# Performance work log

Measured on AMD Instinct MI355X. Metric: run time of the kernel, lower is better.

Reference implementation:

```python
import jax, jax.numpy as jnp
import numpy as np

# distilgpt2 dims
D, NH, HD, NL, V, FF = 768, 12, 64, 6, 50258, 3072
# st-moe dims: Expert hidden = int(768*4*2/3) = 2048 (GEGLU -> first linear out = 4096)
E, TOPN, MOE_H = 8, 2, 2048
CAPF, THRESH, MINCAP, EPS = 1.25, 0.2, 4, 1e-9
BAL_COEF, Z_COEF = 0.01, 0.001
ROUTE_KEY = jax.random.key(1234)  # deterministic stand-in for torch's in-forward uniform_ routing noise


def layer_norm(x, g, b):
    m = jnp.mean(x, -1, keepdims=True)
    v = jnp.mean(jnp.square(x - m), -1, keepdims=True)
    return (x - m) * jax.lax.rsqrt(v + 1e-5) * g + b


def rms_norm(x, g):
    # st-moe RMSNorm: F.normalize(x, dim=-1) * sqrt(dim) * gamma
    n = jnp.sqrt(jnp.sum(jnp.square(x), -1, keepdims=True))
    return x / jnp.maximum(n, 1e-12) * (D ** 0.5) * g


def geglu(h, mult_bias):
    a, gate = jnp.split(h, 2, -1)
    return a * jax.nn.gelu(gate, approximate=False) * mult_bias


def st_ff(x, p):
    # Expert(prenorm=True): RMSNorm -> Linear -> GEGLU -> Linear
    norm_g, w1, b1, mb, w2, b2 = p
    h = rms_norm(x, norm_g)
    return geglu(h @ w1 + b1, mb) @ w2 + b2


def causal_attn(x, wqkv, bqkv, wo, bo):
    B, S, _ = x.shape
    q, k, v = jnp.split(x @ wqkv + bqkv, 3, -1)
    sh = lambda t: t.reshape(B, S, NH, HD).transpose(0, 2, 1, 3)
    q, k, v = sh(q), sh(k), sh(v)
    att = jnp.einsum('bhqd,bhkd->bhqk', q, k) / (HD ** 0.5)
    causal = jnp.tril(jnp.ones((S, S), bool))
    att = jax.nn.softmax(jnp.where(causal, att, jnp.finfo(att.dtype).min), -1)
    o = jnp.einsum('bhqk,bhkd->bhqd', att, v).transpose(0, 2, 1, 3).reshape(B, S, D)
    return o @ wo + bo


def gpt2_mlp(x, wfc, bfc, wproj, bproj):
    # GPT2 uses gelu_new (tanh approximation)
    return jax.nn.gelu(x @ wfc + bfc, approximate=True) @ wproj + bproj


def top_n_gating(x, gate_w, key):
    b, n, _ = x.shape
    cap = max(min(n, int(n * CAPF / E)), MINCAP)
    logits = x @ gate_w                                    # (b,n,E)
    raw = jax.nn.softmax(logits, -1)
    gv, gi = jax.lax.top_k(raw, TOPN)
    gates = jnp.moveaxis(gv, -1, 0)                        # (k,b,n)
    one_hot = jax.nn.one_hot(jnp.moveaxis(gi, -1, 0), E, dtype=x.dtype)  # (k,b,n,E)
    mask1 = one_hot[0]
    gates = gates / jnp.clip(jnp.sum(gates, 0, keepdims=True), EPS)
    thr = jnp.array([EPS, THRESH], x.dtype).reshape(TOPN, 1, 1)
    probs = jax.random.uniform(key, gates.shape, x.dtype)
    route = (probs < gates / thr).at[0].set(True)          # always route to top-1 expert
    mask = one_hot * route[..., None].astype(x.dtype)
    cums = jnp.cumsum(mask, -2) - mask                     # exclusive cumsum over seq
    prev = jnp.zeros((b, 1, E), x.dtype)
    positions, masks = [], []
    for kk in range(TOPN):
        pos = (cums[kk] + prev) * mask[kk]                 # (b,n,E) slot within expert
        mk = mask[kk] * (pos < cap).astype(x.dtype)        # drop overflow beyond capacity
        prev = prev + jnp.sum(mk, -2, keepdims=True)
        positions.append(jnp.sum(pos, -1))                 # (b,n)
        masks.append(mk)
    positions = jnp.stack(positions)                       # (k,b,n)
    mask = jnp.stack(masks)                                # (k,b,n,E)
    mask_flat = jnp.sum(mask, -1)                          # (k,b,n)
    gm = gates * mask_flat * mask_flat
    pos_oh = jax.nn.one_hot(positions.astype(jnp.int32), cap, dtype=x.dtype)  # safe one-hot: OOR -> 0
    combine = jnp.einsum('kbn,kbne,kbnc->bnec', gm, one_hot, pos_oh)
    hard = (combine > 0).astype(x.dtype)
    dispatch = hard + combine - jax.lax.stop_gradient(combine)  # straight-through dispatch
    balance = jnp.mean(jnp.mean(raw, -2) * jnp.mean(mask1, -2)) * float(E ** 2)
    zloss = jnp.mean(jnp.square(jax.nn.logsumexp(logits, -1)))
    return dispatch, combine, balance, zloss


def moe_block(x, ffb, ffa, moe_norm_g, gate_w, ep, key):
    x = st_ff(x, ffb) + x
    res = x
    h = rms_norm(x, moe_norm_g)
    dispatch, combine, bal, zloss = top_n_gating(h, gate_w, key)
    ein = jnp.einsum('bnd,bnec->ebcd', h, dispatch)        # dispatch tokens to experts
    expert = lambda inp, w1, b1, mb, w2, b2: geglu(inp @ w1 + b1, mb) @ w2 + b2
    eout = jax.vmap(expert)(ein, *ep)                      # (E,b,c,d)
    mo = jnp.einsum('ebcd,bnec->bnd', eout, combine)       # weighted combine
    x = mo + res
    x = st_ff(x, ffa) + x
    return x, BAL_COEF * bal + Z_COEF * zloss


def forward(input_ids, wte, wpe, ln1_g, ln1_b, ln2_g, ln2_b, aw, ab, apw, apb, mfw, mfb, mpw, mpb, lnf_g, lnf_b, ffb, ffa, moe_norm_g, gate_w, ep):
    B, S = input_ids.shape
    out = wte[input_ids] + wpe[:S]
    aux = jnp.zeros((), out.dtype)
    for i in range(NL):
        out = out + causal_attn(layer_norm(out, ln1_g[i], ln1_b[i]), aw[i], ab[i], apw[i], apb[i])
        h = layer_norm(out, ln2_g[i], ln2_b[i])
        if i in (0, 3):  # shared SparseMoEBlock replaces MLP (original computes-and-discards the MLP)
            ffo, a = moe_block(h, ffb, ffa, moe_norm_g, gate_w, ep, jax.random.fold_in(ROUTE_KEY, i))
            aux = aux + a
        else:
            ffo = gpt2_mlp(h, mfw[i], mfb[i], mpw[i], mpb[i])
        out = out + ffo
    out = layer_norm(out, lnf_g, lnf_b)
    return out @ wte.T, aux  # tied lm_head


def setup_inputs():
    key = jax.random.key(0)
    ks = iter(jax.random.split(key, 40))
    w = lambda *s: jax.random.normal(next(ks), s, jnp.float32) * 0.02
    B, S = 2, 512
    return dict(
        input_ids=jax.random.randint(next(ks), (B, S), 0, V, jnp.int32),
        attention_mask=jnp.ones((B, S), jnp.int32),
        wte=w(V, D), wpe=w(1024, D),
        ln1_g=jnp.ones((NL, D)), ln1_b=jnp.zeros((NL, D)),
        ln2_g=jnp.ones((NL, D)), ln2_b=jnp.zeros((NL, D)),
        attn_qkv_w=w(NL, D, 3 * D), attn_qkv_b=jnp.zeros((NL, 3 * D)),
        attn_proj_w=w(NL, D, D), attn_proj_b=jnp.zeros((NL, D)),
        mlp_fc_w=w(NL, D, FF), mlp_fc_b=jnp.zeros((NL, FF)),
        mlp_proj_w=w(NL, FF, D), mlp_proj_b=jnp.zeros((NL, D)),
        lnf_g=jnp.ones((D,)), lnf_b=jnp.zeros((D,)),
        ffb_norm_g=jnp.ones((D,)), ffb_w1=w(D, 2 * MOE_H), ffb_b1=jnp.zeros((2 * MOE_H,)), ffb_mb=jnp.ones((MOE_H,)), ffb_w2=w(MOE_H, D), ffb_b2=jnp.zeros((D,)),
        ffa_norm_g=jnp.ones((D,)), ffa_w1=w(D, 2 * MOE_H), ffa_b1=jnp.zeros((2 * MOE_H,)), ffa_mb=jnp.ones((MOE_H,)), ffa_w2=w(MOE_H, D), ffa_b2=jnp.zeros((D,)),
        moe_norm_g=jnp.ones((D,)), gate_w=w(D, E),
        exp_w1=w(E, D, 2 * MOE_H), exp_b1=jnp.zeros((E, 2 * MOE_H)), exp_mb=jnp.ones((E, MOE_H)), exp_w2=w(E, MOE_H, D), exp_b2=jnp.zeros((E, D)),
    )


def reference(input_ids, attention_mask, wte, wpe, ln1_g, ln1_b, ln2_g, ln2_b, attn_qkv_w, attn_qkv_b, attn_proj_w, attn_proj_b, mlp_fc_w, mlp_fc_b, mlp_proj_w, mlp_proj_b, lnf_g, lnf_b, ffb_norm_g, ffb_w1, ffb_b1, ffb_mb, ffb_w2, ffb_b2, ffa_norm_g, ffa_w1, ffa_b1, ffa_mb, ffa_w2, ffa_b2, moe_norm_g, gate_w, exp_w1, exp_b1, exp_mb, exp_w2, exp_b2):
    # attention_mask is built but never used by the original forward (causal-only attention)
    del attention_mask
    return forward(input_ids, wte, wpe, ln1_g, ln1_b, ln2_g, ln2_b,
                   attn_qkv_w, attn_qkv_b, attn_proj_w, attn_proj_b,
                   mlp_fc_w, mlp_fc_b, mlp_proj_w, mlp_proj_b, lnf_g, lnf_b,
                   (ffb_norm_g, ffb_w1, ffb_b1, ffb_mb, ffb_w2, ffb_b2),
                   (ffa_norm_g, ffa_w1, ffa_b1, ffa_mb, ffa_w2, ffa_b2),
                   moe_norm_g, gate_w, (exp_w1, exp_b1, exp_mb, exp_w2, exp_b2))
```

## Files before the change

kernel.cpp:

```cpp
#include <hip/hip_runtime.h>
#include <cstdint>

#define DD     768
#define NTOK   1024
#define SEQ    512
#define NHEAD  12
#define HDIM   64
#define VOCAB  50258
#define CAP    80
#define AUXOFF 51464192LL

typedef short bf16x8 __attribute__((ext_vector_type(8)));
typedef float f32x4  __attribute__((ext_vector_type(4)));

__host__ __device__ inline void threefry(uint32_t k0, uint32_t k1,
                                         uint32_t& x0, uint32_t& x1) {
  uint32_t ks0 = k0, ks1 = k1, ks2 = k0 ^ k1 ^ 0x1BD11BDAu;
  x0 += ks0; x1 += ks1;
#define RND(r) { x0 += x1; x1 = (x1 << (r)) | (x1 >> (32 - (r))); x1 ^= x0; }
  RND(13) RND(15) RND(26) RND(6)   x0 += ks1; x1 += ks2 + 1u;
  RND(17) RND(29) RND(16) RND(24)  x0 += ks2; x1 += ks0 + 2u;
  RND(13) RND(15) RND(26) RND(6)   x0 += ks0; x1 += ks1 + 3u;
  RND(17) RND(29) RND(16) RND(24)  x0 += ks1; x1 += ks2 + 4u;
  RND(13) RND(15) RND(26) RND(6)   x0 += ks2; x1 += ks0 + 5u;
// ... 7 lines not shown
}
__device__ inline float bf2f(unsigned short h) {
  union { uint32_t u; float f; } v; v.u = ((uint32_t)h) << 16; return v.f;
}
__device__ inline float gelu_tanh_f(float x) {
  float x3 = x * x * x;
  return 0.5f * x * (1.f + tanhf(0.7978845608028654f * (x + 0.044715f * x3)));
}
__device__ inline float gelu_erf_f(float x) {
  return 0.5f * x * (1.f + erff(x * 0.7071067811865476f));
}

template<bool TRANS_B>
__global__ __launch_bounds__(256)
void k_gemm(const float* __restrict__ Ag, const float* __restrict__ Bg,
            float* __restrict__ Cg, const float* __restrict__ biasg,
            const float* __restrict__ residg,
            int M, int N, int K, int lda, int ldb, int ldc, int nh,
            long long sAb, long long sAh, long long sBb, long long sBh,
            long long sCb, long long sCh, long long sBias, int act)
{
  const int z  = blockIdx.z;
  const int zb = z / nh, zh = z - zb * nh;
  const float* A = Ag + zb * sAb + zh * sAh;
  const float* B = Bg + zb * sBb + zh * sBh;
  float*       C = Cg + zb * sCb + zh * sCh;
  const float* R = residg ? residg + zb * sCb + zh * sCh : nullptr;
  const float* bs = biasg ? biasg + (long long)z * sBias : nullptr;

  const int m0 = blockIdx.y * 64;
  const int n0 = blockIdx.x * 64;

  __shared__ __attribute__((aligned(16))) unsigned short sAh_[64][36];
  __shared__ __attribute__((aligned(16))) unsigned short sAl_[64][36];
  __shared__ __attribute__((aligned(16))) unsigned short sBh_[64][36];
  __shared__ __attribute__((aligned(16))) unsigned short sBl_[64][36];

  const int tid  = threadIdx.x;
  const int wave = tid >> 6;
  const int lane = tid & 63;
  const int l15  = lane & 15;
  const int kf   = (lane >> 4) * 8;
// ... 78 lines not shown
    __syncthreads();
  }

  #pragma unroll
  for (int f = 0; f < 4; f++) {
    int col = n0 + f * 16 + l15;
    if (col >= N) continue;
    float bv = bs ? bs[col] : 0.f;
    #pragma unroll
    for (int i = 0; i < 4; i++) {
      int row = m0 + wave * 16 + (lane >> 4) * 4 + i;
      if (row >= M) continue;
      float v = acc[f][i] + bv;
      if (act == 1) v = gelu_tanh_f(v);
      if (R) v += R[(long long)row * ldc + col];
      C[(long long)row * ldc + col] = v;
    }
  }
}

__global__ __launch_bounds__(256)
void k_gemmw(const float* __restrict__ Ag, const unsigned short* __restrict__ Bhg,
             const unsigned short* __restrict__ Blg, float* __restrict__ Cg,
             const float* __restrict__ biasg, const float* __restrict__ residg,
             int M, int N, int K, int ldc,
             long long sAz, long long sBz, long long sCz, long long sBias,
             int act, int swz)
{
  const int z = blockIdx.z;
  const float* A = Ag + z * sAz;
  const unsigned short* BH = Bhg + z * sBz;
  const unsigned short* BL = Blg + z * sBz;
  float* C = Cg + z * sCz;
  const float* R = residg ? residg + z * sCz : nullptr;
  const float* bs = biasg ? biasg + z * sBias : nullptr;

  int xt, yt;
  if (swz) {
    int gx = gridDim.x, gy = gridDim.y;
    int bid = blockIdx.y * gx + blockIdx.x;
    int nblk = gx * gy;
    int q = nblk >> 3, r = nblk & 7;
    int xcd = bid & 7, idx = bid >> 3;
    int nl = (xcd < r ? xcd * (q + 1) : r * (q + 1) + (xcd - r) * q) + idx;
    yt = nl % gy; xt = nl / gy;
  } else { xt = blockIdx.x; yt = blockIdx.y; }

  const int m0 = yt * 64, n0 = xt * 128;
// ... 3 lines not shown
  __shared__ __attribute__((aligned(16))) unsigned short sBh[128][40];
  __shared__ __attribute__((aligned(16))) unsigned short sBl[128][40];

  const int tid = threadIdx.x, wave = tid >> 6, lane = tid & 63;
  const int l15 = lane & 15, kf = (lane >> 4) * 8;
  const int wr = (wave >> 1) * 32, wc = (wave & 1) * 64;

  f32x4 zf = {0.f, 0.f, 0.f, 0.f};
  f32x4 acc[2][4] = {{zf, zf, zf, zf}, {zf, zf, zf, zf}};

  const int ar = tid >> 2, ac = (tid & 3) * 8;
  const int br = tid >> 1, bc = (tid & 1) * 16;

  for (int kk = 0; kk < K; kk += 32) {
    {
      float v[8];
      if (m0 + ar < M) {
        const float* p = A + (long long)(m0 + ar) * K + kk + ac;
        #pragma unroll
        for (int j = 0; j < 8; j++) v[j] = p[j];
      } else {
        #pragma unroll
        for (int j = 0; j < 8; j++) v[j] = 0.f;
      }
      #pragma unroll
      for (int j = 0; j < 8; j += 4) {
        unsigned short h0 = f2bf(v[j]),     h1 = f2bf(v[j + 1]);
        unsigned short h2 = f2bf(v[j + 2]), h3 = f2bf(v[j + 3]);
        uint2 ph, pl;
        ph.x = (uint32_t)h0 | ((uint32_t)h1 << 16);
        ph.y = (uint32_t)h2 | ((uint32_t)h3 << 16);
        pl.x = (uint32_t)f2bf(v[j] - bf2f(h0))     | ((uint32_t)f2bf(v[j + 1] - bf2f(h1)) << 16);
        pl.y = (uint32_t)f2bf(v[j + 2] - bf2f(h2)) | ((uint32_t)f2bf(v[j + 3] - bf2f(h3)) << 16);
        *(uint2*)&sAh[ar][ac + j] = ph;
        *(uint2*)&sAl[ar][ac + j] = pl;
      }
    }
    {
      int nrow = n0 + br;
      if (nrow < N) {
        const uint4* ph = (const uint4*)(BH + (long long)nrow * K + kk + bc);
        const uint4* pl = (const uint4*)(BL + (long long)nrow * K + kk + bc);
        *(uint4*)&sBh[br][bc]     = ph[0];
        *(uint4*)&sBh[br][bc + 8] = ph[1];
        *(uint4*)&sBl[br][bc]     = pl[0];
        *(uint4*)&sBl[br][bc + 8] = pl[1];
      } else {
        uint4 z4 = {0, 0, 0, 0};
        *(uint4*)&sBh[br][bc] = z4; *(uint4*)&sBh[br][bc + 8] = z4;
        *(uint4*)&sBl[br][bc] = z4; *(uint4*)&sBl[br][bc + 8] = z4;
// ... 12 lines not shown
    #pragma unroll
    for (int j = 0; j < 4; j++) {
      union { uint4 q; bf16x8 v; } ub, ulb;
      ub.q  = *(const uint4*)&sBh[wc + j * 16 + l15][kf];
      ulb.q = *(const uint4*)&sBl[wc + j * 16 + l15][kf];
      #pragma unroll
      for (int i = 0; i < 2; i++) {
        acc[i][j] = __builtin_amdgcn_mfma_f32_16x16x32_bf16(ah[i], ub.v,  acc[i][j], 0, 0, 0);
        acc[i][j] = __builtin_amdgcn_mfma_f32_16x16x32_bf16(al[i], ub.v,  acc[i][j], 0, 0, 0);
        acc[i][j] = __builtin_amdgcn_mfma_f32_16x16x32_bf16(ah[i], ulb.v, acc[i][j], 0, 0, 0);
      }
    }
    __syncthreads();
  }

  #pragma unroll
  for (int j = 0; j < 4; j++) {
    int col = n0 + wc + j * 16 + l15;
    if (col >= N) continue;
    float bv = bs ? bs[col] : 0.f;
    #pragma unroll
    for (int i = 0; i < 2; i++) {
      #pragma unroll
      for (int rr = 0; rr < 4; rr++) {
        int row = m0 + wr + i * 16 + (lane >> 4) * 4 + rr;
        if (row >= M) continue;
        float v = acc[i][j][rr] + bv;
        if (act == 1) v = gelu_tanh_f(v);
        if (R) v += R[(long long)row * ldc + col];
        C[(long long)row * ldc + col] = v;
      }
    }
  }
}

__global__ void k_split(const float* __restrict__ src, unsigned short* __restrict__ dh,
                        unsigned short* __restrict__ dl, long long n) {
  long long i = ((long long)blockIdx.x * 256 + threadIdx.x) * 4;
  if (i >= n) return;
  float4 v = *(const float4*)(src + i);
  float vv[4] = {v.x, v.y, v.z, v.w};
  unsigned short h[4], l[4];
  #pragma unroll
  for (int j = 0; j < 4; j++) {
    h[j] = f2bf(vv[j]);
// ... 26 lines not shown
  }
}

__global__ void k_embed(const int* __restrict__ ids, const float* __restrict__ wte,
                        const float* __restrict__ wpe, float* __restrict__ X) {
  int t = blockIdx.x; int s = t & (SEQ - 1);
  long long wb = (long long)ids[t] * DD;
  #pragma unroll
  for (int i = 0; i < 3; i++) {
    int d = threadIdx.x + 256 * i;
    X[(long long)t * DD + d] = wte[wb + d] + wpe[(long long)s * DD + d];
  }
}

__global__ void k_layernorm(const float* __restrict__ in, const float* __restrict__ g,
                            const float* __restrict__ b, float* __restrict__ out) {
  int t = blockIdx.x; int lane = threadIdx.x;
  float xv[12]; float s = 0.f, ss = 0.f;
  #pragma unroll
  for (int i = 0; i < 12; i++) {
    xv[i] = in[(long long)t * DD + lane + 64 * i];
    s += xv[i]; ss += xv[i] * xv[i];
  }
  for (int o = 32; o; o >>= 1) { s += __shfl_xor(s, o); ss += __shfl_xor(ss, o); }
  float mean = s * (1.f / DD);
  float var  = ss * (1.f / DD) - mean * mean;
  float rst  = rsqrtf(var + 1e-5f);
  #pragma unroll
  for (int i = 0; i < 12; i++) {
    int d = lane + 64 * i;
    out[(long long)t * DD + d] = (xv[i] - mean) * rst * g[d] + b[d];
  }
}

__global__ void k_rmsnorm(const float* __restrict__ in, const float* __restrict__ g,
                          float* __restrict__ out) {
  int t = blockIdx.x; int lane = threadIdx.x;
  float xv[12]; float ss = 0.f;
  #pragma unroll
  for (int i = 0; i < 12; i++) {
    xv[i] = in[(long long)t * DD + lane + 64 * i];
    ss += xv[i] * xv[i];
  }
  for (int o = 32; o; o >>= 1) ss += __shfl_xor(ss, o);
  float scale = 27.712812921102035f / fmaxf(sqrtf(ss), 1e-12f);
  #pragma unroll
  for (int i = 0; i < 12; i++) {
    int d = lane + 64 * i;
    out[(long long)t * DD + d] = xv[i] * scale * g[d];
  }
}

__global__ void k_softmax(float* __restrict__ S) {
  int r = blockIdx.x; int q = r & (SEQ - 1);
  float* p = S + (long long)r * SEQ;
  int lane = threadIdx.x;
  float v[8]; float mx = -3.4e38f;
  #pragma unroll
  for (int i = 0; i < 8; i++) {
    int j = lane + 64 * i;
    v[i] = p[j] * 0.125f;
    if (j <= q) mx = fmaxf(mx, v[i]);
  }
  for (int o = 32; o; o >>= 1) mx = fmaxf(mx, __shfl_xor(mx, o));
  float s = 0.f;
  #pragma unroll
  for (int i = 0; i < 8; i++) {
    int j = lane + 64 * i;
    float e = (j <= q) ? expf(v[i] - mx) : 0.f;
    v[i] = e; s += e;
  }
  for (int o = 32; o; o >>= 1) s += __shfl_xor(s, o);
  float inv = 1.f / s;
  #pragma unroll
  for (int i = 0; i < 8; i++) p[lane + 64 * i] = v[i] * inv;
}

__global__ void k_geglu(const float* __restrict__ in, const float* __restrict__ mb,
                        float* __restrict__ out, int rows_per_mb) {
  int row = blockIdx.x;
  const float* mbp = mb + (long long)(row / rows_per_mb) * 2048;
  #pragma unroll
  for (int i = 0; i < 8; i++) {
    int j = threadIdx.x + 256 * i;
    float a = in[(long long)row * 4096 + j];
    float g = in[(long long)row * 4096 + 2048 + j];
    out[(long long)row * 2048 + j] = a * gelu_erf_f(g) * mbp[j];
  }
}

__global__ void k_zero(float* __restrict__ p, int n) {
  int i = blockIdx.x * blockDim.x + threadIdx.x;
  if (i < n) p[i] = 0.f;
}

__global__ void k_add(float* __restrict__ X, const float* __restrict__ Y, int n) {
  int i = blockIdx.x * 256 + threadIdx.x;
  if (i < n) X[i] += Y[i];
}

__global__ void k_gate(const float* __restrict__ RB, const float* __restrict__ GW,
                       unsigned int fk0, unsigned int fk1,
// ... 38 lines not shown
    uint32_t x0 = (uint32_t)t, x1 = (uint32_t)t + 1024u;
    threefry(fk0, fk1, x0, x1);
    union { uint32_t u; float f; } uf; uf.u = (x1 >> 9) | 0x3f800000u;
    float u = uf.f - 1.f;
    int r1 = (u < g1 * 5.f) ? 1 : 0;
    e0a[t] = e0; e1a[t] = e1; g0a[t] = g0; g1a[t] = g1; r1a[t] = r1;
    atomicAdd(&cnt1[b * 8 + e0], 1.f);
    atomicAdd(lse2, lse * lse);
  }
}

__global__ void k_scan(const int* __restrict__ e0a, const int* __restrict__ e1a,
                       const int* __restrict__ r1a,
                       int* __restrict__ s0a, int* __restrict__ s1a,
                       int* __restrict__ ts) {
  int tid = threadIdx.x;
  if (tid >= 16) return;
  int b = tid >> 3, e = tid & 7;
  int base = (e * 2 + b) * CAP;
  for (int c = 0; c < CAP; c++) ts[base + c] = -1;
  int c0 = 0;
  for (int n = 0; n < SEQ; n++) {
    int t = b * SEQ + n;
    if (e0a[t] == e) {
      if (c0 < CAP) { s0a[t] = c0; ts[base + c0] = t; } else s0a[t] = -1;
      c0++;
    }
  }
  int prev = c0 < CAP ? c0 : CAP;
  int c1 = 0;
  for (int n = 0; n < SEQ; n++) {
    int t = b * SEQ + n;
    if (e1a[t] == e) {
      if (r1a[t]) {
        int pos = prev + c1;
        if (pos < CAP) { s1a[t] = pos; ts[base + pos] = t; } else s1a[t] = -1;
        c1++;
      } else s1a[t] = -1;
    }
  }
}

__global__ void k_dispatch(const float* __restrict__ RB, const int* __restrict__ ts,
                           float* __restrict__ EIN) {
  int s = blockIdx.x;
  int t = ts[s];
  #pragma unroll
  for (int i = 0; i < 3; i++) {
    int d = threadIdx.x + 256 * i;
    EIN[(long long)s * DD + d] = (t >= 0) ? RB[(long long)t * DD + d] : 0.f;
  }
}

__global__ void k_combine(const int* __restrict__ e0a, const int* __restrict__ e1a,
                          const int* __restrict__ s0a, const int* __restrict__ s1a,
                          const float* __restrict__ g0a, const float* __restrict__ g1a,
                          const float* __restrict__ EOUT, float* __restrict__ XM) {
  int t = blockIdx.x; int b = t >> 9;
  int s0 = s0a[t], s1 = s1a[t];
  long long r0 = ((long long)e0a[t] * 160 + b * CAP + s0) * DD;
  long long r1 = ((long long)e1a[t] * 160 + b * CAP + s1) * DD;
  float g0 = g0a[t], g1 = g1a[t];
  #pragma unroll
  for (int i = 0; i < 3; i++) {
    int d = threadIdx.x + 256 * i;
// ... 45 lines not shown
  const float* ffaw1 = (const float*)d_in[25];
  const float* ffab1 = (const float*)d_in[26];
  const float* ffamb = (const float*)d_in[27];
  const float* ffaw2 = (const float*)d_in[28];
  const float* ffab2 = (const float*)d_in[29];
  const float* moeng = (const float*)d_in[30];
  const float* gw    = (const float*)d_in[31];
  const float* ew1   = (const float*)d_in[32];
  const float* eb1   = (const float*)d_in[33];
  const float* emb   = (const float*)d_in[34];
  const float* ew2   = (const float*)d_in[35];
  const float* eb2   = (const float*)d_in[36];

  float* ws = (float*)d_ws;
  float* X    = ws + 0;
  float* LN   = ws + 786432;
  float* RB   = ws + 1572864;
  float* XM   = ws + 2359296;
  float* QKV  = ws + 3145728;
  float* BIG  = ws + 5505024;
  float* GB   = ws + 11796480;
  float* EIN  = ws + 14417920;
  float* EOUT = ws + 15400960;
  float* MISC = ws + 16384000;
  int*   e0a = (int*)MISC;
  int*   e1a = e0a + 1024;
  int*   s0a = e1a + 1024;
  int*   s1a = s0a + 1024;
  int*   r1a = s1a + 1024;
  float* g0a = (float*)(r1a + 1024);
  float* g1a = g0a + 1024;
  int*   tsa = (int*)(g1a + 1024);
  float* sum_raw = (float*)(tsa + 1280);
  float* cnt1 = sum_raw + 16;
  float* lse2 = cnt1 + 16;

  float* logits = (float*)d_out;
  float* aux = logits + AUXOFF;

  const long long E_wte = 38598144LL, E_qkv = 1769472LL, E_apr = 589824LL;
  const long long E_fc = 2359296LL, E_mpr = 2359296LL;
  const long long E_fb1 = 3145728LL, E_fb2 = 1572864LL;
  const long long E_ew1 = 3145728LL, E_ew2 = 1572864LL;
  const long long o_wte = 0;
  const long long o_qkv = o_wte + 2 * E_wte;
  const long long o_apr = o_qkv + 12 * E_qkv;
  const long long o_fc  = o_apr + 12 * E_apr;
  const long long o_mpr = o_fc  + 8 * E_fc;
  const long long o_fb1 = o_mpr + 8 * E_mpr;
  const long long o_fb2 = o_fb1 + 2 * E_fb1;
  const long long o_fa1 = o_fb2 + 2 * E_fb2;
  const long long o_fa2 = o_fa1 + 2 * E_fb1;
  const long long o_ew1 = o_fa2 + 2 * E_fb2;
  const long long o_ew2 = o_ew1 + 16 * E_ew1;
  const long long o_end = o_ew2 + 16 * E_ew2;
  unsigned short* SP = (unsigned short*)(ws + 16400000);
  const bool useSplit = ((long long)ws_size >= 16400000LL * 4 + o_end * 2);

  unsigned int fk[2][2];
  { uint32_t a = 0, b = 0; threefry(0u, 1234u, a, b); fk[0][0] = a; fk[0][1] = b; }
  { uint32_t a = 0, b = 3; threefry(0u, 1234u, a, b); fk[1][0] = a; fk[1][1] = b; }

  auto gemm = [&](bool transB, const float* A, const float* Bm, float* Cm,
                  const float* bias, const float* resid,
                  int M, int N, int K, int lda, int ldb, int ldc,
                  int batches, int nh,
                  long long sAb, long long sAh, long long sBb, long long sBh,
                  long long sCb, long long sCh, long long sBias, int act) {
    dim3 g((N + 63) / 64, (M + 63) / 64, batches);
    if (transB)
      k_gemm<true><<<g, 256, 0, stream>>>(A, Bm, Cm, bias, resid, M, N, K, lda, ldb, ldc,
                                          nh, sAb, sAh, sBb, sBh, sCb, sCh, sBias, act);
    else
      k_gemm<false><<<g, 256, 0, stream>>>(A, Bm, Cm, bias, resid, M, N, K, lda, ldb, ldc,
                                           nh, sAb, sAh, sBb, sBh, sCb, sCh, sBias, act);
  };

  auto wgemm = [&](const float* A, const float* Bf, long long bOff, long long bE,
                   float* Cm, const float* bias, const float* resid,
                   int M, int N, int K, int ldc, int nz,
                   long long sAz, long long sBf, long long sCz, long long sBias,
                   int act, int swz) {
    if (useSplit) {
      dim3 g((N + 127) / 128, (M + 63) / 64, nz);
      k_gemmw<<<g, 256, 0, stream>>>(A, SP + bOff, SP + bOff + bE, Cm, bias, resid,
                                     M, N, K, ldc, sAz, 2 * bE, sCz, sBias, act, swz);
    } else {
      gemm(false, A, Bf, Cm, bias, resid, M, N, K, K, N, ldc,
           nz, 1, sAz, 0, sBf, 0, sCz, 0, sBias, act);
    }
  };

  if (useSplit) {
    auto splitT = [&](const float* src, long long dOff, long long E, int K_, int N_,
                      int nz, long long sSrc) {
      k_split_t<<<dim3(N_ / 32, K_ / 32, nz), 256, 0, stream>>>(
          src, SP + dOff, SP + dOff + E, K_, N_, sSrc, 2 * E);
    };
    k_split<<<(int)((E_wte / 4 + 255) / 256), 256, 0, stream>>>(
        wte, SP + o_wte, SP + o_wte + E_wte, E_wte);
    splitT(aqw, o_qkv, E_qkv, 768, 2304, 6, 768LL * 2304);
    splitT(apw, o_apr, E_apr, 768, 768, 6, 768LL * 768);
    int mlpLayers[4] = {1, 2, 4, 5};
    for (int s = 0; s < 4; s++) {
      int L = mlpLayers[s];
      splitT(mfw + (long long)L * E_fc,  o_fc  + s * 2 * E_fc,  E_fc,  768, 3072, 1, 0);
      splitT(mpw + (long long)L * E_mpr, o_mpr + s * 2 * E_mpr, E_mpr, 3072, 768, 1, 0);
    }
    splitT(ffbw1, o_fb1, E_fb1, 768, 4096, 1, 0);
    splitT(ffbw2, o_fb2, E_fb2, 2048, 768, 1, 0);
    splitT(ffaw1, o_fa1, E_fb1, 768, 4096, 1, 0);
    splitT(ffaw2, o_fa2, E_fb2, 2048, 768, 1, 0);
    splitT(ew1, o_ew1, E_ew1, 768, 4096, 8, (long long)768 * 4096);
    splitT(ew2, o_ew2, E_ew2, 2048, 768, 8, (long long)2048 * 768);
  }

  auto moe = [&](unsigned int fk0, unsigned int fk1) {
    k_rmsnorm<<<1024, 64, 0, stream>>>(LN, ffbng, RB);
    wgemm(RB, ffbw1, o_fb1, E_fb1, BIG, ffbb1, nullptr,
          1024, 4096, 768, 4096, 1, 0, 0, 0, 0, 0, 1);
    k_geglu<<<1024, 256, 0, stream>>>(BIG, ffbmb, GB, 1024);
    wgemm(GB, ffbw2, o_fb2, E_fb2, XM, ffbb2, LN,
          1024, 768, 2048, 768, 1, 0, 0, 0, 0, 0, 1);
    k_rmsnorm<<<1024, 64, 0, stream>>>(XM, moeng, RB);
    k_zero<<<1, 64, 0, stream>>>(sum_raw, 33);
    k_gate<<<1024, 64, 0, stream>>>(RB, gw, fk0, fk1, e0a, e1a, g0a, g1a, r1a,
                                    sum_raw, cnt1, lse2);
    k_scan<<<1, 64, 0, stream>>>(e0a, e1a, r1a, s0a, s1a, tsa);
    k_dispatch<<<1280, 256, 0, stream>>>(RB, tsa, EIN);
    wgemm(EIN, ew1, o_ew1, E_ew1, BIG, eb1, nullptr,
          160, 4096, 768, 4096, 8, 122880, 3145728, 655360, 4096, 0, 0);
    k_geglu<<<1280, 256, 0, stream>>>(BIG, emb, GB, 160);
    wgemm(GB, ew2, o_ew2, E_ew2, EOUT, eb2, nullptr,
          160, 768, 2048, 768, 8, 327680, 1572864, 122880, 768, 0, 0);
    k_combine<<<1024, 256, 0, stream>>>(e0a, e1a, s0a, s1a, g0a, g1a, EOUT, XM);
    k_aux<<<1, 1, 0, stream>>>(sum_raw, cnt1, lse2, aux);
    k_rmsnorm<<<1024, 64, 0, stream>>>(XM, ffang, RB);
    wgemm(RB, ffaw1, o_fa1, E_fb1, BIG, ffab1, nullptr,
          1024, 4096, 768, 4096, 1, 0, 0, 0, 0, 0, 1);
    k_geglu<<<1024, 256, 0, stream>>>(BIG, ffamb, GB, 1024);
    wgemm(GB, ffaw2, o_fa2, E_fb2, XM, ffab2, XM,
          1024, 768, 2048, 768, 1, 0, 0, 0, 0, 0, 1);
    k_add<<<3072, 256, 0, stream>>>(X, XM, 786432);
  };

  k_zero<<<1, 64, 0, stream>>>(aux, 1);
  k_embed<<<1024, 256, 0, stream>>>(ids, wte, wpe, X);

  for (int i = 0; i < 6; i++) {
    k_layernorm<<<1024, 64, 0, stream>>>(X, ln1g + i * 768, ln1b + i * 768, LN);
    wgemm(LN, aqw + (long long)i * 768 * 2304, o_qkv + (long long)i * 2 * E_qkv, E_qkv,
          QKV, aqb + (long long)i * 2304, nullptr,
          1024, 2304, 768, 2304, 1, 0, 0, 0, 0, 0, 1);
    gemm(true, QKV, QKV + 768, BIG, nullptr, nullptr, 512, 512, 64, 2304, 2304, 512,
         24, 12, 1179648, 64, 1179648, 64, 3145728, 262144, 0, 0);
    k_softmax<<<12288, 64, 0, stream>>>(BIG);
    gemm(false, BIG, QKV + 1536, GB, nullptr, nullptr, 512, 64, 512, 512, 2304, 768,
         24, 12, 3145728, 262144, 1179648, 64, 393216, 64, 0, 0);
    wgemm(GB, apw + (long long)i * 768 * 768, o_apr + (long long)i * 2 * E_apr, E_apr,
          X, apb + (long long)i * 768, X,
          1024, 768, 768, 768, 1, 0, 0, 0, 0, 0, 1);
    k_layernorm<<<1024, 64, 0, stream>>>(X, ln2g + i * 768, ln2b + i * 768, LN);
    if (i == 0 || i == 3) {
      moe(fk[i == 0 ? 0 : 1][0], fk[i == 0 ? 0 : 1][1]);
    } else {
      int slot = (i < 3) ? (i - 1) : (i - 2);
      wgemm(LN, mfw + (long long)i * 768 * 3072, o_fc + (long long)slot * 2 * E_fc, E_fc,
            BIG, mfb + (long long)i * 3072, nullptr,
            1024, 3072, 768, 3072, 1, 0, 0, 0, 0, 1, 1);
      wgemm(BIG, mpw + (long long)i * 3072 * 768, o_mpr + (long long)slot * 2 * E_mpr, E_mpr,
            X, mpb + (long long)i * 768, X,
            1024, 768, 3072, 768, 1, 0, 0, 0, 0, 0, 1);
    }
  }

  k_layernorm<<<1024, 64, 0, stream>>>(X, lnfg, lnfb, LN);
  if (useSplit) {
    wgemm(LN, nullptr, o_wte, E_wte, logits, nullptr, nullptr,
          1024, VOCAB, 768, VOCAB, 1, 0, 0, 0, 0, 0, 1);
  } else {
    gemm(true, LN, wte, logits, nullptr, nullptr, 1024, VOCAB, 768, 768, 768, VOCAB,
         1, 1, 0, 0, 0, 0, 0, 0, 0, 0);
  }
}
```

Measured before the change: 4.412 ms.

## Emit pre-split bf16 hi/lo activations from producers to skip GEMM A-side conversion

Result: faster. 4.134 ms (-6.3%).

```diff
diff --git a/kernel.cpp b/kernel.cpp
--- a/kernel.cpp
+++ b/kernel.cpp
@@ -45,18 +45,19 @@
 template<bool TRANS_B>
 __global__ __launch_bounds__(256)
 void k_gemm(const float* __restrict__ Ag, const float* __restrict__ Bg,
-            float* __restrict__ Cg, const float* __restrict__ biasg,
-            const float* __restrict__ residg,
+            float* __restrict__ Cg, unsigned short* __restrict__ Chg,
+            unsigned short* __restrict__ Clg,
+            const float* __restrict__ biasg, const float* __restrict__ residg,
             int M, int N, int K, int lda, int ldb, int ldc, int nh,
             long long sAb, long long sAh, long long sBb, long long sBh,
-            long long sCb, long long sCh, long long sBias, int act)
+            long long sCb, long long sCh, long long sBias, int act, int osplit)
 {
   const int z  = blockIdx.z;
   const int zb = z / nh, zh = z - zb * nh;
   const float* A = Ag + zb * sAb + zh * sAh;
   const float* B = Bg + zb * sBb + zh * sBh;
-  float*       C = Cg + zb * sCb + zh * sCh;
-  const float* R = residg ? residg + zb * sCb + zh * sCh : nullptr;
+  const long long cOff = zb * sCb + zh * sCh;
+  const float* R = residg ? residg + cOff : nullptr;
   const float* bs = biasg ? biasg + (long long)z * sBias : nullptr;
 
   const int m0 = blockIdx.y * 64;
@@ -165,24 +166,33 @@
       float v = acc[f][i] + bv;
       if (act == 1) v = gelu_tanh_f(v);
       if (R) v += R[(long long)row * ldc + col];
-      C[(long long)row * ldc + col] = v;
+      long long idx = cOff + (long long)row * ldc + col;
+      if (osplit) {
+        unsigned short h = f2bf(v);
+        Chg[idx] = h;
+        Clg[idx] = f2bf(v - bf2f(h));
+      } else {
+        Cg[idx] = v;
+      }
     }
   }
 }
 
 __global__ __launch_bounds__(256)
-void k_gemmw(const float* __restrict__ Ag, const unsigned short* __restrict__ Bhg,
-             const unsigned short* __restrict__ Blg, float* __restrict__ Cg,
+void k_gemmw(const unsigned short* __restrict__ Ahg, const unsigned short* __restrict__ Alg,
+             const unsigned short* __restrict__ Bhg, const unsigned short* __restrict__ Blg,
+             float* __restrict__ Cg, unsigned short* __restrict__ Chg,
+             unsigned short* __restrict__ Clg,
              const float* __restrict__ biasg, const float* __restrict__ residg,
              int M, int N, int K, int ldc,
              long long sAz, long long sBz, long long sCz, long long sBias,
              int act, int swz)
 {
   const int z = blockIdx.z;
-  const float* A = Ag + z * sAz;
+  const unsigned short* AH = Ahg + z * sAz;
+  const unsigned short* AL = Alg + z * sAz;
   const unsigned short* BH = Bhg + z * sBz;
   const unsigned short* BL = Blg + z * sBz;
-  float* C = Cg + z * sCz;
   const float* R = residg ? residg + z * sCz : nullptr;
   const float* bs = biasg ? biasg + z * sBias : nullptr;
 
@@ -216,26 +226,14 @@
 
   for (int kk = 0; kk < K; kk += 32) {
     {
-      float v[8];
       if (m0 + ar < M) {
-        const float* p = A + (long long)(m0 + ar) * K + kk + ac;
-        #pragma unroll
-        for (int j = 0; j < 8; j++) v[j] = p[j];
+        long long o = (long long)(m0 + ar) * K + kk + ac;
+        *(uint4*)&sAh[ar][ac] = *(const uint4*)(AH + o);
+        *(uint4*)&sAl[ar][ac] = *(const uint4*)(AL + o);
       } else {
-        #pragma unroll
-        for (int j = 0; j < 8; j++) v[j] = 0.f;
-      }
-      #pragma unroll
-      for (int j = 0; j < 8; j += 4) {
-        unsigned short h0 = f2bf(v[j]),     h1 = f2bf(v[j + 1]);
-        unsigned short h2 = f2bf(v[j + 2]), h3 = f2bf(v[j + 3]);
-        uint2 ph, pl;
-        ph.x = (uint32_t)h0 | ((uint32_t)h1 << 16);
-        ph.y = (uint32_t)h2 | ((uint32_t)h3 << 16);
-        pl.x = (uint32_t)f2bf(v[j] - bf2f(h0))     | ((uint32_t)f2bf(v[j + 1] - bf2f(h1)) << 16);
-        pl.y = (uint32_t)f2bf(v[j + 2] - bf2f(h2)) | ((uint32_t)f2bf(v[j + 3] - bf2f(h3)) << 16);
-        *(uint2*)&sAh[ar][ac + j] = ph;
-        *(uint2*)&sAl[ar][ac + j] = pl;
+        uint4 z4 = {0, 0, 0, 0};
+        *(uint4*)&sAh[ar][ac] = z4;
+        *(uint4*)&sAl[ar][ac] = z4;
       }
     }
     {
@@ -278,6 +276,7 @@
     __syncthreads();
   }
 
+  const int osplit = (Chg != nullptr);
   #pragma unroll
   for (int j = 0; j < 4; j++) {
     int col = n0 + wc + j * 16 + l15;
@@ -292,7 +291,14 @@
         float v = acc[i][j][rr] + bv;
         if (act == 1) v = gelu_tanh_f(v);
         if (R) v += R[(long long)row * ldc + col];
-        C[(long long)row * ldc + col] = v;
+        long long idx = (long long)z * sCz + (long long)row * ldc + col;
+        if (osplit) {
+          unsigned short h = f2bf(v);
+          Chg[idx] = h;
+          Clg[idx] = f2bf(v - bf2f(h));
+        } else {
+          Cg[idx] = v;
+        }
       }
     }
   }
@@ -349,7 +355,8 @@
 }
 
 __global__ void k_layernorm(const float* __restrict__ in, const float* __restrict__ g,
-                            const float* __restrict__ b, float* __restrict__ out) {
+                            const float* __restrict__ b, float* __restrict__ out,
+                            unsigned short* __restrict__ oh, unsigned short* __restrict__ ol) {
   int t = blockIdx.x; int lane = threadIdx.x;
   float xv[12]; float s = 0.f, ss = 0.f;
   #pragma unroll
@@ -364,12 +371,20 @@
   #pragma unroll
   for (int i = 0; i < 12; i++) {
     int d = lane + 64 * i;
-    out[(long long)t * DD + d] = (xv[i] - mean) * rst * g[d] + b[d];
+    float y = (xv[i] - mean) * rst * g[d] + b[d];
+    long long idx = (long long)t * DD + d;
+    out[idx] = y;
+    if (oh) {
+      unsigned short h = f2bf(y);
+      oh[idx] = h;
+      ol[idx] = f2bf(y - bf2f(h));
+    }
   }
 }
 
 __global__ void k_rmsnorm(const float* __restrict__ in, const float* __restrict__ g,
-                          float* __restrict__ out) {
+                          float* __restrict__ out,
+                          unsigned short* __restrict__ oh, unsigned short* __restrict__ ol) {
   int t = blockIdx.x; int lane = threadIdx.x;
   float xv[12]; float ss = 0.f;
   #pragma unroll
@@ -382,7 +397,14 @@
   #pragma unroll
   for (int i = 0; i < 12; i++) {
     int d = lane + 64 * i;
-    out[(long long)t * DD + d] = xv[i] * scale * g[d];
+    float y = xv[i] * scale * g[d];
+    long long idx = (long long)t * DD + d;
+    out[idx] = y;
+    if (oh) {
+      unsigned short h = f2bf(y);
+      oh[idx] = h;
+      ol[idx] = f2bf(y - bf2f(h));
+    }
   }
 }
 
@@ -412,7 +434,8 @@
 }
 
 __global__ void k_geglu(const float* __restrict__ in, const float* __restrict__ mb,
-                        float* __restrict__ out, int rows_per_mb) {
+                        float* __restrict__ outf, unsigned short* __restrict__ oh,
+                        unsigned short* __restrict__ ol, int rows_per_mb) {
   int row = blockIdx.x;
   const float* mbp = mb + (long long)(row / rows_per_mb) * 2048;
   #pragma unroll
@@ -420,7 +443,15 @@
     int j = threadIdx.x + 256 * i;
     float a = in[(long long)row * 4096 + j];
     float g = in[(long long)row * 4096 + 2048 + j];
-    out[(long long)row * 2048 + j] = a * gelu_erf_f(g) * mbp[j];
+    float y = a * gelu_erf_f(g) * mbp[j];
+    long long idx = (long long)row * 2048 + j;
+    if (oh) {
+      unsigned short h = f2bf(y);
+      oh[idx] = h;
+      ol[idx] = f2bf(y - bf2f(h));
+    } else {
+      outf[idx] = y;
+    }
   }
 }
 
@@ -489,7 +520,12 @@
                        const int* __restrict__ r1a,
                        int* __restrict__ s0a, int* __restrict__ s1a,
                        int* __restrict__ ts) {
+  __shared__ int se0[NTOK], se1[NTOK], sr1[NTOK];
   int tid = threadIdx.x;
+  for (int i = tid; i < NTOK; i += 64) {
+    se0[i] = e0a[i]; se1[i] = e1a[i]; sr1[i] = r1a[i];
+  }
+  __syncthreads();
   if (tid >= 16) return;
   int b = tid >> 3, e = tid & 7;
   int base = (e * 2 + b) * CAP;
@@ -497,7 +533,7 @@
   int c0 = 0;
   for (int n = 0; n < SEQ; n++) {
     int t = b * SEQ + n;
-    if (e0a[t] == e) {
+    if (se0[t] == e) {
       if (c0 < CAP) { s0a[t] = c0; ts[base + c0] = t; } else s0a[t] = -1;
       c0++;
     }
@@ -506,8 +542,8 @@
   int c1 = 0;
   for (int n = 0; n < SEQ; n++) {
     int t = b * SEQ + n;
-    if (e1a[t] == e) {
-      if (r1a[t]) {
+    if (se1[t] == e) {
+      if (sr1[t]) {
         int pos = prev + c1;
         if (pos < CAP) { s1a[t] = pos; ts[base + pos] = t; } else s1a[t] = -1;
         c1++;
@@ -524,6 +560,26 @@
   for (int i = 0; i < 3; i++) {
     int d = threadIdx.x + 256 * i;
     EIN[(long long)s * DD + d] = (t >= 0) ? RB[(long long)t * DD + d] : 0.f;
+  }
+}
+
+__global__ void k_dispatch_s(const unsigned short* __restrict__ RBh,
+                             const unsigned short* __restrict__ RBl,
+                             const int* __restrict__ ts,
+                             unsigned short* __restrict__ Eh,
+                             unsigned short* __restrict__ El) {
+  int s = blockIdx.x;
+  int t = ts[s];
+  #pragma unroll
+  for (int i = 0; i < 3; i++) {
+    int d = threadIdx.x + 256 * i;
+    long long o = (long long)s * DD + d;
+    if (t >= 0) {
+      long long src = (long long)t * DD + d;
+      Eh[o] = RBh[src]; El[o] = RBl[src];
+    } else {
+      Eh[o] = 0; El[o] = 0;
+    }
   }
 }
 
@@ -599,8 +655,8 @@
 
   float* ws = (float*)d_ws;
   float* X    = ws + 0;
-  float* LN   = ws + 786432;
-  float* RB   = ws + 1572864;
+  float* LNf  = ws + 786432;
+  float* RBf  = ws + 1572864;
   float* XM   = ws + 2359296;
   float* QKV  = ws + 3145728;
   float* BIG  = ws + 5505024;
@@ -620,6 +676,19 @@
   float* cnt1 = sum_raw + 16;
   float* lse2 = cnt1 + 16;
 
+  unsigned short* LNh = (unsigned short*)(ws + 2359296);
+  unsigned short* LNl = LNh + 786432;
+  unsigned short* Oh  = LNh;
+  unsigned short* Ol  = LNl;
+  unsigned short* RBh = (unsigned short*)(ws + 3145728);
+  unsigned short* RBl = RBh + 786432;
+  unsigned short* Hh  = (unsigned short*)(ws + 5505024);
+  unsigned short* Hl  = Hh + 3145728;
+  unsigned short* GBh = (unsigned short*)(ws + 11796480);
+  unsigned short* GBl = GBh + 2621440;
+  unsigned short* EINh = (unsigned short*)(ws + 14417920);
+  unsigned short* EINl = EINh + 983040;
+
   float* logits = (float*)d_out;
   float* aux = logits + AUXOFF;
 
@@ -647,34 +716,37 @@
   { uint32_t a = 0, b = 3; threefry(0u, 1234u, a, b); fk[1][0] = a; fk[1][1] = b; }
 
   auto gemm = [&](bool transB, const float* A, const float* Bm, float* Cm,
+                  unsigned short* Ch, unsigned short* Cl,
                   const float* bias, const float* resid,
                   int M, int N, int K, int lda, int ldb, int ldc,
                   int batches, int nh,
                   long long sAb, long long sAh, long long sBb, long long sBh,
-                  long long sCb, long long sCh, long long sBias, int act) {
+                  long long sCb, long long sCh, long long sBias, int act, int osplit) {
     dim3 g((N + 63) / 64, (M + 63) / 64, batches);
     if (transB)
-      k_gemm<true><<<g, 256, 0, stream>>>(A, Bm, Cm, bias, resid, M, N, K, lda, ldb, ldc,
-                                          nh, sAb, sAh, sBb, sBh, sCb, sCh, sBias, act);
+      k_gemm<true><<<g, 256, 0, stream>>>(A, Bm, Cm, Ch, Cl, bias, resid, M, N, K,
+                                          lda, ldb, ldc, nh, sAb, sAh, sBb, sBh,
+                                          sCb, sCh, sBias, act, osplit);
     else
-      k_gemm<false><<<g, 256, 0, stream>>>(A, Bm, Cm, bias, resid, M, N, K, lda, ldb, ldc,
-                                           nh, sAb, sAh, sBb, sBh, sCb, sCh, sBias, act);
+      k_gemm<false><<<g, 256, 0, stream>>>(A, Bm, Cm, Ch, Cl, bias, resid, M, N, K,
+                                           lda, ldb, ldc, nh, sAb, sAh, sBb, sBh,
+                                           sCb, sCh, sBias, act, osplit);
   };
 
-  auto wgemm = [&](const float* A, const float* Bf, long long bOff, long long bE,
-                   float* Cm, const float* bias, const float* resid,
-                   int M, int N, int K, int ldc, int nz,
-                   long long sAz, long long sBf, long long sCz, long long sBias,
-                   int act, int swz) {
-    if (useSplit) {
-      dim3 g((N + 127) / 128, (M + 63) / 64, nz);
-      k_gemmw<<<g, 256, 0, stream>>>(A, SP + bOff, SP + bOff + bE, Cm, bias, resid,
-                                     M, N, K, ldc, sAz, 2 * bE, sCz, sBias, act, swz);
-    } else {
-      gemm(false, A, Bf, Cm, bias, resid, M, N, K, K, N, ldc,
-           nz, 1, sAz, 0, sBf, 0, sCz, 0, sBias, act);
-    }
+  auto wg = [&](const unsigned short* Ah_, const unsigned short* Al_,
+                long long bOff, long long bE,
+                float* Cf, unsigned short* Ch, unsigned short* Cl,
+                const float* bias, const float* resid,
+                int M, int N, int K, int ldc, int nz,
+                long long sAz, long long sCz, long long sBias, int act, int swz) {
+    dim3 g((N + 127) / 128, (M + 63) / 64, nz);
+    k_gemmw<<<g, 256, 0, stream>>>(Ah_, Al_, SP + bOff, SP + bOff + bE, Cf, Ch, Cl,
+                                   bias, resid, M, N, K, ldc, sAz, 2 * bE, sCz,
+                                   sBias, act, swz);
   };
+
+  k_zero<<<1, 64, 0, stream>>>(aux, 1);
+  k_embed<<<1024, 256, 0, stream>>>(ids, wte, wpe, X);
 
   if (useSplit) {
     auto splitT = [&](const float* src, long long dOff, long long E, int K_, int N_,
@@ -698,73 +770,125 @@
     splitT(ffaw2, o_fa2, E_fb2, 2048, 768, 1, 0);
     splitT(ew1, o_ew1, E_ew1, 768, 4096, 8, (long long)768 * 4096);
     splitT(ew2, o_ew2, E_ew2, 2048, 768, 8, (long long)2048 * 768);
-  }
-
-  auto moe = [&](unsigned int fk0, unsigned int fk1) {
-    k_rmsnorm<<<1024, 64, 0, stream>>>(LN, ffbng, RB);
-    wgemm(RB, ffbw1, o_fb1, E_fb1, BIG, ffbb1, nullptr,
-          1024, 4096, 768, 4096, 1, 0, 0, 0, 0, 0, 1);
-    k_geglu<<<1024, 256, 0, stream>>>(BIG, ffbmb, GB, 1024);
-    wgemm(GB, ffbw2, o_fb2, E_fb2, XM, ffbb2, LN,
-          1024, 768, 2048, 768, 1, 0, 0, 0, 0, 0, 1);
-    k_rmsnorm<<<1024, 64, 0, stream>>>(XM, moeng, RB);
-    k_zero<<<1, 64, 0, stream>>>(sum_raw, 33);
-    k_gate<<<1024, 64, 0, stream>>>(RB, gw, fk0, fk1, e0a, e1a, g0a, g1a, r1a,
-                                    sum_raw, cnt1, lse2);
-    k_scan<<<1, 64, 0, stream>>>(e0a, e1a, r1a, s0a, s1a, tsa);
-    k_dispatch<<<1280, 256, 0, stream>>>(RB, tsa, EIN);
-    wgemm(EIN, ew1, o_ew1, E_ew1, BIG, eb1, nullptr,
-          160, 4096, 768, 4096, 8, 122880, 3145728, 655360, 4096, 0, 0);
-    k_geglu<<<1280, 256, 0, stream>>>(BIG, emb, GB, 160);
-    wgemm(GB, ew2, o_ew2, E_ew2, EOUT, eb2, nullptr,
-          160, 768, 2048, 768, 8, 327680, 1572864, 122880, 768, 0, 0);
-    k_combine<<<1024, 256, 0, stream>>>(e0a, e1a, s0a, s1a, g0a, g1a, EOUT, XM);
-    k_aux<<<1, 1, 0, stream>>>(sum_raw, cnt1, lse2, aux);
-    k_rmsnorm<<<1024, 64, 0, stream>>>(XM, ffang, RB);
-    wgemm(RB, ffaw1, o_fa1, E_fb1, BIG, ffab1, nullptr,
-          1024, 4096, 768, 4096, 1, 0, 0, 0, 0, 0, 1);
-    k_geglu<<<1024, 256, 0, stream>>>(BIG, ffamb, GB, 1024);
-    wgemm(GB, ffaw2, o_fa2, E_fb2, XM, ffab2, XM,
-          1024, 768, 2048, 768, 1, 0, 0, 0, 0, 0, 1);
-    k_add<<<3072, 256, 0, stream>>>(X, XM, 786432);
-  };
-
-  k_zero<<<1, 64, 0, stream>>>(aux, 1);
-  k_embed<<<1024, 256, 0, stream>>>(ids, wte, wpe, X);
-
-  for (int i = 0; i < 6; i++) {
-    k_layernorm<<<1024, 64, 0, stream>>>(X, ln1g + i * 768, ln1b + i * 768, LN);
-    wgemm(LN, aqw + (long long)i * 768 * 2304, o_qkv + (long long)i * 2 * E_qkv, E_qkv,
-          QKV, aqb + (long long)i * 2304, nullptr,
-          1024, 2304, 768, 2304, 1, 0, 0, 0, 0, 0, 1);
-    gemm(true, QKV, QKV + 768, BIG, nullptr, nullptr, 512, 512, 64, 2304, 2304, 512,
-         24, 12, 1179648, 64, 1179648, 64, 3145728, 262144, 0, 0);
-    k_softmax<<<12288, 64, 0, stream>>>(BIG);
-    gemm(false, BIG, QKV + 1536, GB, nullptr, nullptr, 512, 64, 512, 512, 2304, 768,
-         24, 12, 3145728, 262144, 1179648, 64, 393216, 64, 0, 0);
-    wgemm(GB, apw + (long long)i * 768 * 768, o_apr + (long long)i * 2 * E_apr, E_apr,
-          X, apb + (long long)i * 768, X,
-          1024, 768, 768, 768, 1, 0, 0, 0, 0, 0, 1);
-    k_layernorm<<<1024, 64, 0, stream>>>(X, ln2g + i * 768, ln2b + i * 768, LN);
-    if (i == 0 || i == 3) {
-      moe(fk[i == 0 ? 0 : 1][0], fk[i == 0 ? 0 : 1][1]);
-    } else {
-      int slot = (i < 3) ? (i - 1) : (i - 2);
-      wgemm(LN, mfw + (long long)i * 768 * 3072, o_fc + (long long)slot * 2 * E_fc, E_fc,
-            BIG, mfb + (long long)i * 3072, nullptr,
-            1024, 3072, 768, 3072, 1, 0, 0, 0, 0, 1, 1);
-      wgemm(BIG, mpw + (long long)i * 3072 * 768, o_mpr + (long long)slot * 2 * E_mpr, E_mpr,
-            X, mpb + (long long)i * 768, X,
-            1024, 768, 3072, 768, 1, 0, 0, 0, 0, 0, 1);
-    }
-  }
-
-  k_layernorm<<<1024, 64, 0, stream>>>(X, lnfg, lnfb, LN);
-  if (useSplit) {
-    wgemm(LN, nullptr, o_wte, E_wte, logits, nullptr, nullptr,
-          1024, VOCAB, 768, VOCAB, 1, 0, 0, 0, 0, 0, 1);
+
+    auto moe = [&](unsigned int fk0, unsigned int fk1) {
+      k_rmsnorm<<<1024, 64, 0, stream>>>(LNf, ffbng, RBf, RBh, RBl);
+      wg(RBh, RBl, o_fb1, E_fb1, BIG, nullptr, nullptr, ffbb1, nullptr,
+         1024, 4096, 768, 4096, 1, 0, 0, 0, 0, 1);
+      k_geglu<<<1024, 256, 0, stream>>>(BIG, ffbmb, nullptr, GBh, GBl, 1024);
+      wg(GBh, GBl, o_fb2, E_fb2, XM, nullptr, nullptr, ffbb2, LNf,
+         1024, 768, 2048, 768, 1, 0, 0, 0, 0, 1);
+      k_rmsnorm<<<1024, 64, 0, stream>>>(XM, moeng, RBf, RBh, RBl);
+      k_zero<<<1, 64, 0, stream>>>(sum_raw, 33);
+      k_gate<<<1024, 64, 0, stream>>>(RBf, gw, fk0, fk1, e0a, e1a, g0a, g1a, r1a,
+                                      sum_raw, cnt1, lse2);
+      k_scan<<<1, 64, 0, stream>>>(e0a, e1a, r1a, s0a, s1a, tsa);
+      k_dispatch_s<<<1280, 256, 0, stream>>>(RBh, RBl, tsa, EINh, EINl);
+      wg(EINh, EINl, o_ew1, E_ew1, BIG, nullptr, nullptr, eb1, nullptr,
+         160, 4096, 768, 4096, 8, 122880, 655360, 4096, 0, 0);
+      k_geglu<<<1280, 256, 0, stream>>>(BIG, emb, nullptr, GBh, GBl, 160);
+      wg(GBh, GBl, o_ew2, E_ew2, EOUT, nullptr, nullptr, eb2, nullptr,
+         160, 768, 2048, 768, 8, 327680, 122880, 768, 0, 0);
+      k_combine<<<1024, 256, 0, stream>>>(e0a, e1a, s0a, s1a, g0a, g1a, EOUT, XM);
+      k_aux<<<1, 1, 0, stream>>>(sum_raw, cnt1, lse2, aux);
+      k_rmsnorm<<<1024, 64, 0, stream>>>(XM, ffang, RBf, RBh, RBl);
+      wg(RBh, RBl, o_fa1, E_fb1, BIG, nullptr, nullptr, ffab1, nullptr,
+         1024, 4096, 768, 4096, 1, 0, 0, 0, 0, 1);
+      k_geglu<<<1024, 256, 0, stream>>>(BIG, ffamb, nullptr, GBh, GBl, 1024);
+      wg(GBh, GBl, o_fa2, E_fb2, XM, nullptr, nullptr, ffab2, XM,
+         1024, 768, 2048, 768, 1, 0, 0, 0, 0, 1);
+      k_add<<<3072, 256, 0, stream>>>(X, XM, 786432);
+    };
+
+    for (int i = 0; i < 6; i++) {
+      k_layernorm<<<1024, 64, 0, stream>>>(X, ln1g + i * 768, ln1b + i * 768, LNf, LNh, LNl);
+      wg(LNh, LNl, o_qkv + (long long)i * 2 * E_qkv, E_qkv, QKV, nullptr, nullptr,
+         aqb + (long long)i * 2304, nullptr, 1024, 2304, 768, 2304, 1, 0, 0, 0, 0, 1);
+      gemm(true, QKV, QKV + 768, BIG, nullptr, nullptr, nullptr, nullptr,
+           512, 512, 64, 2304, 2304, 512, 24, 12,
+           1179648, 64, 1179648, 64, 3145728, 262144, 0, 0, 0);
+      k_softmax<<<12288, 64, 0, stream>>>(BIG);
+      gemm(false, BIG, QKV + 1536, nullptr, Oh, Ol, nullptr, nullptr,
+           512, 64, 512, 512, 2304, 768, 24, 12,
+           3145728, 262144, 1179648, 64, 393216, 64, 0, 0, 1);
+      wg(Oh, Ol, o_apr + (long long)i * 2 * E_apr, E_apr, X, nullptr, nullptr,
+         apb + (long long)i * 768, X, 1024, 768, 768, 768, 1, 0, 0, 0, 0, 1);
+      k_layernorm<<<1024, 64, 0, stream>>>(X, ln2g + i * 768, ln2b + i * 768, LNf, LNh, LNl);
+      if (i == 0 || i == 3) {
+        moe(fk[i == 0 ? 0 : 1][0], fk[i == 0 ? 0 : 1][1]);
+      } else {
+        int slot = (i < 3) ? (i - 1) : (i - 2);
+        wg(LNh, LNl, o_fc + (long long)slot * 2 * E_fc, E_fc, nullptr, Hh, Hl,
+           mfb + (long long)i * 3072, nullptr, 1024, 3072, 768, 3072, 1, 0, 0, 0, 1, 1);
+        wg(Hh, Hl, o_mpr + (long long)slot * 2 * E_mpr, E_mpr, X, nullptr, nullptr,
+           mpb + (long long)i * 768, X, 1024, 768, 3072, 768, 1, 0, 0, 0, 0, 1);
+      }
+    }
+
+    k_layernorm<<<1024, 64, 0, stream>>>(X, lnfg, lnfb, LNf, LNh, LNl);
+    wg(LNh, LNl, o_wte, E_wte, logits, nullptr, nullptr, nullptr, nullptr,
+       1024, VOCAB, 768, VOCAB, 1, 0, 0, 0, 0, 1);
   } else {
-    gemm(true, LN, wte, logits, nullptr, nullptr, 1024, VOCAB, 768, 768, 768, VOCAB,
-         1, 1, 0, 0, 0, 0, 0, 0, 0, 0);
-  }
-}
+    auto moe = [&](unsigned int fk0, unsigned int fk1) {
+      k_rmsnorm<<<1024, 64, 0, stream>>>(LNf, ffbng, RBf, nullptr, nullptr);
+      gemm(false, RBf, ffbw1, BIG, nullptr, nullptr, ffbb1, nullptr, 1024, 4096, 768,
+           768, 4096, 4096, 1, 1, 0, 0, 0, 0, 0, 0, 0, 0, 0);
+      k_geglu<<<1024, 256, 0, stream>>>(BIG, ffbmb, GB, nullptr, nullptr, 1024);
+      gemm(false, GB, ffbw2, XM, nullptr, nullptr, ffbb2, LNf, 1024, 768, 2048,
+           2048, 768, 768, 1, 1, 0, 0, 0, 0, 0, 0, 0, 0, 0);
+      k_rmsnorm<<<1024, 64, 0, stream>>>(XM, moeng, RBf, nullptr, nullptr);
+      k_zero<<<1, 64, 0, stream>>>(sum_raw, 33);
+      k_gate<<<1024, 64, 0, stream>>>(RBf, gw, fk0, fk1, e0a, e1a, g0a, g1a, r1a,
+                                      sum_raw, cnt1, lse2);
+      k_scan<<<1, 64, 0, stream>>>(e0a, e1a, r1a, s0a, s1a, tsa);
+      k_dispatch<<<1280, 256, 0, stream>>>(RBf, tsa, EIN);
+      gemm(false, EIN, ew1, BIG, nullptr, nullptr, eb1, nullptr, 160, 4096, 768,
+           768, 4096, 4096, 8, 1, 122880, 0, 3145728, 0, 655360, 0, 4096, 0, 0);
+      k_geglu<<<1280, 256, 0, stream>>>(BIG, emb, GB, nullptr, nullptr, 160);
+      gemm(false, GB, ew2, EOUT, nullptr, nullptr, eb2, nullptr, 160, 768, 2048,
+           2048, 768, 768, 8, 1, 327680, 0, 1572864, 0, 122880, 0, 768, 0, 0);
+      k_combine<<<1024, 256, 0, stream>>>(e0a, e1a, s0a, s1a, g0a, g1a, EOUT, XM);
+      k_aux<<<1, 1, 0, stream>>>(sum_raw, cnt1, lse2, aux);
+      k_rmsnorm<<<1024, 64, 0, stream>>>(XM, ffang, RBf, nullptr, nullptr);
+      gemm(false, RBf, ffaw1, BIG, nullptr, nullptr, ffab1, nullptr, 1024, 4096, 768,
+           768, 4096, 4096, 1, 1, 0, 0, 0, 0, 0, 0, 0, 0, 0);
+      k_geglu<<<1024, 256, 0, stream>>>(BIG, ffamb, GB, nullptr, nullptr, 1024);
+      gemm(false, GB, ffaw2, XM, nullptr, nullptr, ffab2, XM, 1024, 768, 2048,
+           2048, 768, 768, 1, 1, 0, 0, 0, 0, 0, 0, 0, 0, 0);
+      k_add<<<3072, 256, 0, stream>>>(X, XM, 786432);
+    };
+
+    for (int i = 0; i < 6; i++) {
+      k_layernorm<<<1024, 64, 0, stream>>>(X, ln1g + i * 768, ln1b + i * 768, LNf,
+                                           nullptr, nullptr);
+      gemm(false, LNf, aqw + (long long)i * 768 * 2304, QKV, nullptr, nullptr,
+           aqb + (long long)i * 2304, nullptr, 1024, 2304, 768, 768, 2304, 2304,
+           1, 1, 0, 0, 0, 0, 0, 0, 0, 0, 0);
+      gemm(true, QKV, QKV + 768, BIG, nullptr, nullptr, nullptr, nullptr,
+           512, 512, 64, 2304, 2304, 512, 24, 12,
+           1179648, 64, 1179648, 64, 3145728, 262144, 0, 0, 0);
+      k_softmax<<<12288, 64, 0, stream>>>(BIG);
+      gemm(false, BIG, QKV + 1536, GB, nullptr, nullptr, nullptr, nullptr,
+           512, 64, 512, 512, 2304, 768, 24, 12,
+           3145728, 262144, 1179648, 64, 393216, 64, 0, 0, 0);
+      gemm(false, GB, apw + (long long)i * 768 * 768, X, nullptr, nullptr,
+           apb + (long long)i * 768, X, 1024, 768, 768, 768, 768, 768,
+           1, 1, 0, 0, 0, 0, 0, 0, 0, 0, 0);
+      k_layernorm<<<1024, 64, 0, stream>>>(X, ln2g + i * 768, ln2b + i * 768, LNf,
+                                           nullptr, nullptr);
+      if (i == 0 || i == 3) {
+        moe(fk[i == 0 ? 0 : 1][0], fk[i == 0 ? 0 : 1][1]);
+      } else {
+        gemm(false, LNf, mfw + (long long)i * 768 * 3072, BIG, nullptr, nullptr,
+             mfb + (long long)i * 3072, nullptr, 1024, 3072, 768, 768, 3072, 3072,
+             1, 1, 0, 0, 0, 0, 0, 0, 0, 1, 0);
+        gemm(false, BIG, mpw + (long long)i * 3072 * 768, X, nullptr, nullptr,
+             mpb + (long long)i * 768, X, 1024, 768, 3072, 3072, 768, 768,
+             1, 1, 0, 0, 0, 0, 0, 0, 0, 0, 0);
+      }
+    }
+    k_layernorm<<<1024, 64, 0, stream>>>(X, lnfg, lnfb, LNf, nullptr, nullptr);
+    gemm(true, LNf, wte, logits, nullptr, nullptr, nullptr, nullptr,
+         1024, VOCAB, 768, 768, 768, VOCAB, 1, 1, 0, 0, 0, 0, 0, 0, 0, 0, 0);
+  }
+}
```
